# Kernel tuning notes

Hardware: AMD Instinct MI355X
Metric: run time of the kernel (lower is better)

The kernel has to match this reference:

```python
import jax, jax.numpy as jnp
import numpy as np

D_MODEL = 768
D_LAT = 384
N_FREQ = D_MODEL // 2 + 1  # 385
INIT_S = 0.02


def _quat_linear(x, Ww, Wx, Wy, Wz, b):
    # Ww..Wz: [out_q, in_q]; x: [..., 4*in_q]
    d = Ww.shape[1]
    xw, xx, xy, xz = x[..., :d], x[..., d:2*d], x[..., 2*d:3*d], x[..., 3*d:]
    lin = lambda W, v: jnp.einsum('...i,oi->...o', v, W)
    ow = lin(Ww, xw) - lin(Wx, xx) - lin(Wy, xy) - lin(Wz, xz)
    ox = lin(Ww, xx) + lin(Wx, xw) + lin(Wy, xz) - lin(Wz, xy)
    oy = lin(Ww, xy) - lin(Wx, xz) + lin(Wy, xw) + lin(Wz, xx)
    oz = lin(Ww, xz) + lin(Wx, xy) - lin(Wy, xx) + lin(Wz, xw)
    return jnp.concatenate([ow, ox, oy, oz], axis=-1) + b


def _filter1d(x, kr, ki, n):
    X = jnp.fft.rfft(x, axis=-1)
    K = kr + 1j * ki
    return jnp.fft.irfft(X * K, n=n, axis=-1)


def setup_inputs() -> dict:
    key = jax.random.key(0)
    ks = jax.random.split(key, 16)
    rn = lambda k, shape: jax.random.normal(k, shape, dtype=jnp.float32)
    in_q_e, out_q_e = D_MODEL // 4, D_LAT // 4   # 192, 96
    in_q_d, out_q_d = D_LAT // 4, D_MODEL // 4   # 96, 192
    return {
        'x': rn(ks[0], (8, 4096, D_MODEL)),
        'enc_kr': rn(ks[1], (N_FREQ,)) * INIT_S,
        'enc_ki': rn(ks[2], (N_FREQ,)) * INIT_S,
        'dec_kr': rn(ks[3], (N_FREQ,)) * INIT_S,
        'dec_ki': rn(ks[4], (N_FREQ,)) * INIT_S,
        'enc_Ww': rn(ks[5], (out_q_e, in_q_e)) * 0.02,
        'enc_Wx': rn(ks[6], (out_q_e, in_q_e)) * 0.02,
        'enc_Wy': rn(ks[7], (out_q_e, in_q_e)) * 0.02,
        'enc_Wz': rn(ks[8], (out_q_e, in_q_e)) * 0.02,
        'enc_b': jnp.zeros((D_LAT,), jnp.float32),
        'dec_Ww': rn(ks[9], (out_q_d, in_q_d)) * 0.02,
        'dec_Wx': rn(ks[10], (out_q_d, in_q_d)) * 0.02,
        'dec_Wy': rn(ks[11], (out_q_d, in_q_d)) * 0.02,
        'dec_Wz': rn(ks[12], (out_q_d, in_q_d)) * 0.02,
        'dec_b': jnp.zeros((D_MODEL,), jnp.float32),
    }


def reference(x, enc_kr, enc_ki, dec_kr, dec_ki,
              enc_Ww, enc_Wx, enc_Wy, enc_Wz, enc_b,
              dec_Ww, dec_Wx, dec_Wy, dec_Wz, dec_b):
    # encode: spectral filter -> GELU (exact erf, matching nn.GELU) -> quaternion proj
    h = jax.nn.gelu(_filter1d(x, enc_kr, enc_ki, D_MODEL), approximate=False)
    z = _quat_linear(h, enc_Ww, enc_Wx, enc_Wy, enc_Wz, enc_b)
    # decode: quaternion proj -> spectral filter
    recon = _filter1d(_quat_linear(z, dec_Ww, dec_Wx, dec_Wy, dec_Wz, dec_b),
                      dec_kr, dec_ki, D_MODEL)
    loss = jnp.mean((recon - jax.lax.stop_gradient(x)) ** 2)
    return z, loss
```

## Files before the change

### kernel.cpp

```cpp
#include <hip/hip_runtime.h>
#include <hip/hip_bf16.h>
#include <math.h>

typedef unsigned short u16;
typedef __attribute__((ext_vector_type(8))) short s8v;
typedef __attribute__((ext_vector_type(4))) float f4v;

#define DM 768
#define DL 384

__device__ __forceinline__ u16 f2bf(float f) {
  union { float f; unsigned u; } v; v.f = f;
  unsigned r = v.u + 0x7fffu + ((v.u >> 16) & 1u);
  return (u16)(r >> 16);
}

__global__ void k_build_c2(const float* __restrict__ kr0, const float* __restrict__ ki0,
                           const float* __restrict__ kr1, const float* __restrict__ ki1,
                           float* __restrict__ c0, float* __restrict__ c1) {
  const float* kr = blockIdx.y ? kr1 : kr0;
  const float* ki = blockIdx.y ? ki1 : ki0;
  float* c = blockIdx.y ? c1 : c0;
  const int t = blockIdx.x;
  const int f = threadIdx.x;
  float s = 0.f;
  for (int ff = f; ff < 384; ff += 256) {
    if (ff >= 1) {
      int ph = (ff * t) % DM;
      float th = (float)ph * (6.283185307179586f / DM);
      float sn, cs; sincosf(th, &sn, &cs);
      s += 2.f * (kr[ff] * cs - ki[ff] * sn);
    }
  }
  if (f == 0) s += kr[0] + ((t & 1) ? -kr[384] : kr[384]);
  __shared__ float red[256];
  red[f] = s; __syncthreads();
  for (int k = 128; k > 0; k >>= 1) {
    if (f < k) red[f] += red[f + k];
    __syncthreads();
  }
  if (f == 0) c[t] = red[0] * (1.f / DM);
}

__global__ void k_rb2(const float* __restrict__ c, const float* __restrict__ b,
                      float* __restrict__ rb) {
  const int i = blockIdx.x;
  const int f = threadIdx.x;
  float s = 0.f;
  for (int j = f; j < DM; j += 256) {
    int ci = i - j; if (ci < 0) ci += DM;
    s += c[ci] * b[j];
  }
  __shared__ float red[256];
  red[f] = s; __syncthreads();
  for (int k = 128; k > 0; k >>= 1) {
    if (f < k) red[f] += red[f + k];
    __syncthreads();
  }
  if (f == 0) rb[i] = red[0];
}

__device__ __constant__ int   MI_[4][4] = {{0,1,2,3},{1,0,3,2},{2,3,0,1},{3,2,1,0}};
__device__ __constant__ float SG_[4][4] = {{1,-1,-1,-1},{1,1,-1,1},{1,1,1,-1},{1,-1,1,1}};

__global__ void k_static(const float* __restrict__ c_enc, u16* __restrict__ Benc,
                         const float* __restrict__ c_dec, u16* __restrict__ Cdec,
                         const float* __restrict__ eWw, const float* __restrict__ eWx,
                         const float* __restrict__ eWy, const float* __restrict__ eWz,
                         u16* __restrict__ Wenc,
                         const float* __restrict__ dWw, const float* __restrict__ dWx,
                         const float* __restrict__ dWy, const float* __restrict__ dWz,
                         u16* __restrict__ DdT) {
  const int b = blockIdx.x;
  const int tt = threadIdx.x;
  if (b < 4608) {
    const float* c = (b < 2304) ? c_enc : c_dec;
    u16* B = (b < 2304) ? Benc : Cdec;
    int idx = (b < 2304 ? b : b - 2304) * 256 + tt;
    int i = idx / DM, j = idx % DM;
    int d = i - j; if (d < 0) d += DM;
    B[idx] = f2bf(c[d]);
  } else if (b < 5760) {
    int idx = (b - 4608) * 256 + tt;
    int o = idx / DM, j = idx % DM;
    int p = o / 96, r = o % 96, q = j / 192, cc = j % 192;
    const float* Ws[4] = {eWw, eWx, eWy, eWz};
    Wenc[idx] = f2bf(SG_[p][q] * Ws[MI_[p][q]][r * 192 + cc]);
  } else {
    int idx = (b - 5760) * 256 + tt;
    int o = idx / DM, j = idx % DM;
    int p = j / 192, r = j % 192, q = o / 96, cc = o % 96;
    const float* Ws[4] = {dWw, dWx, dWy, dWz};
    DdT[idx] = f2bf(SG_[p][q] * Ws[MI_[p][q]][r * 96 + cc]);
  }
}

__device__ __forceinline__ void ld_lds16(const u16* g, u16* l) {
  __builtin_amdgcn_global_load_lds((const __attribute__((address_space(1))) void*)g,
                                   (__attribute__((address_space(3))) void*)l, 16, 0, 0);
}

__global__ __launch_bounds__(512, 1) void gemm8f_g1(
    const float* __restrict__ X, const u16* __restrict__ B, u16* __restrict__ outb) {
  __shared__ __align__(16) u16 SM[57344];
  const int t = threadIdx.x;
  const int lane = t & 63, wid = t >> 6;
  const int wrow = wid >> 2, wcol = wid & 3;
  int wg = blockIdx.x;
  { const int q = gridDim.x >> 3; wg = (wg & 7) * q + (wg >> 3); }
  const int bm = wg >> 2, bn = wg & 3;
  constexpr int KT = 768, NT = 768, NKT = KT / 64;

  f4v acc[8][3];
#pragma unroll
  for (int m = 0; m < 8; ++m)
#pragma unroll
    for (int n = 0; n < 3; ++n) acc[m][n] = (f4v)0.f;

  const int srow = t >> 3;
  const int sgrp = (t & 7) ^ (srow & 7);
  const float* gX = X + (size_t)(bm * 256 + srow) * KT + sgrp * 8;
  const u16*   gB = B + (size_t)(bn * 192 + srow) * KT + sgrp * 8;
  const int sx = ((lane >> 4) ^ (lane & 7)) * 8;
  const int ar = (wrow * 128 + (lane & 15)) * 64;
  const int br = 32768 + (wcol * 48 + (lane & 15)) * 64;

  auto stgB = [&](int kt_, int c_) {
    const u16* g = gB + (size_t)(c_ * 64) * KT + kt_ * 64;
    ld_lds16(g, SM + 32768 + (kt_ & 1) * 12288 + c_ * 4096 + t * 8);
  };
  float4 ra0[4], ra1[4];
  auto LA = [&](int kt_, int half_, float4* r) {
    const float* g = gX + (size_t)(half_ * 128) * KT + kt_ * 64;
    r[0] = *(const float4*)(g);
    r[1] = *(const float4*)(g + 4);
    r[2] = *(const float4*)(g + 64 * KT);
    r[3] = *(const float4*)(g + 64 * KT + 4);
  };
  auto WA = [&](int kt_, int half_, const float4* r) {
    union { u16 u[8]; s8v s; } w0, w1;
    w0.u[0] = f2bf(r[0].x); w0.u[1] = f2bf(r[0].y);
    w0.u[2] = f2bf(r[0].z); w0.u[3] = f2bf(r[0].w);
    w0.u[4] = f2bf(r[1].x); w0.u[5] = f2bf(r[1].y);
    w0.u[6] = f2bf(r[1].z); w0.u[7] = f2bf(r[1].w);
    w1.u[0] = f2bf(r[2].x); w1.u[1] = f2bf(r[2].y);
    w1.u[2] = f2bf(r[2].z); w1.u[3] = f2bf(r[2].w);
    w1.u[4] = f2bf(r[3].x); w1.u[5] = f2bf(r[3].y);
    w1.u[6] = f2bf(r[3].z); w1.u[7] = f2bf(r[3].w);
    u16* l = SM + (kt_ & 1) * 16384 + half_ * 8192 + t * 8;
    *(s8v*)l = w0.s;
    *(s8v*)(l + 4096) = w1.s;
  };

  stgB(0, 0); stgB(0, 1); stgB(0, 2);
  LA(0, 0, ra0); LA(0, 1, ra1);
  asm volatile("s_waitcnt vmcnt(4)" ::: "memory");
  __builtin_amdgcn_sched_barrier(0);
  WA(0, 0, ra0);
  asm volatile("s_waitcnt vmcnt(0)" ::: "memory");
  __builtin_amdgcn_sched_barrier(0);
  WA(0, 1, ra1);
  asm volatile("s_waitcnt lgkmcnt(0)" ::: "memory");
  __builtin_amdgcn_sched_barrier(0);
  __builtin_amdgcn_s_barrier();

#pragma unroll 2
  for (int kt = 0; kt < NKT; ++kt) {
    const int ca = (kt & 1) * 16384;
    const int cbb = (kt & 1) * 12288;
    s8v a0[4][2], a1[4][2], b01[2][2], b2[2];
#pragma unroll
    for (int m = 0; m < 4; ++m) {
      a0[m][0] = *(const s8v*)(SM + ca + ar + m * 1024 + sx);
      a0[m][1] = *(const s8v*)(SM + ca + ar + m * 1024 + (sx ^ 32));
    }
#pragma unroll
    for (int n = 0; n < 2; ++n) {
      b01[n][0] = *(const s8v*)(SM + cbb + br + n * 1024 + sx);
      b01[n][1] = *(const s8v*)(SM + cbb + br + n * 1024 + (sx ^ 32));
    }
    if (kt + 1 < NKT) {
      stgB(kt + 1, 0); stgB(kt + 1, 1); stgB(kt + 1, 2);
      LA(kt + 1, 0, ra0);
      LA(kt + 1, 1, ra1);
    }
    __builtin_amdgcn_s_barrier();
    asm volatile("s_waitcnt lgkmcnt(0)" ::: "memory");
    __builtin_amdgcn_sched_barrier(0);
    __builtin_amdgcn_s_setprio(1);
#pragma unroll
    for (int m = 0; m < 4; ++m)
#pragma unroll
      for (int n = 0; n < 2; ++n) {
        acc[m][n] = __builtin_amdgcn_mfma_f32_16x16x32_bf16(a0[m][0], b01[n][0], acc[m][n], 0, 0, 0);
        acc[m][n] = __builtin_amdgcn_mfma_f32_16x16x32_bf16(a0[m][1], b01[n][1], acc[m][n], 0, 0, 0);
      }
    __builtin_amdgcn_s_setprio(0);
    __builtin_amdgcn_s_barrier();
#pragma unroll
    for (int m = 0; m < 4; ++m) {
      a1[m][0] = *(const s8v*)(SM + ca + ar + (4 + m) * 1024 + sx);
      a1[m][1] = *(const s8v*)(SM + ca + ar + (4 + m) * 1024 + (sx ^ 32));
    }
    __builtin_amdgcn_s_barrier();
    asm volatile("s_waitcnt lgkmcnt(0)" ::: "memory");
    __builtin_amdgcn_sched_barrier(0);
    __builtin_amdgcn_s_setprio(1);
#pragma unroll
    for (int m = 0; m < 4; ++m)
#pragma unroll
      for (int n = 0; n < 2; ++n) {
        acc[4 + m][n] = __builtin_amdgcn_mfma_f32_16x16x32_bf16(a1[m][0], b01[n][0], acc[4 + m][n], 0, 0, 0);
        acc[4 + m][n] = __builtin_amdgcn_mfma_f32_16x16x32_bf16(a1[m][1], b01[n][1], acc[4 + m][n], 0, 0, 0);
      }
    __builtin_amdgcn_s_setprio(0);
    __builtin_amdgcn_s_barrier();
    b2[0] = *(const s8v*)(SM + cbb + br + 2048 + sx);
    b2[1] = *(const s8v*)(SM + cbb + br + 2048 + (sx ^ 32));
    if (kt + 1 < NKT) {
      asm volatile("s_waitcnt vmcnt(4)" ::: "memory");
      __builtin_amdgcn_sched_barrier(0);
      WA(kt + 1, 0, ra0);
    }
    __builtin_amdgcn_s_barrier();
    asm volatile("s_waitcnt lgkmcnt(0)" ::: "memory");
    __builtin_amdgcn_sched_barrier(0);
    __builtin_amdgcn_s_setprio(1);
#pragma unroll
    for (int m = 0; m < 4; ++m) {
      acc[4 + m][2] = __builtin_amdgcn_mfma_f32_16x16x32_bf16(a1[m][0], b2[0], acc[4 + m][2], 0, 0, 0);
      acc[4 + m][2] = __builtin_amdgcn_mfma_f32_16x16x32_bf16(a1[m][1], b2[1], acc[4 + m][2], 0, 0, 0);
    }
    __builtin_amdgcn_s_setprio(0);
    __builtin_amdgcn_s_barrier();
    if (kt + 1 < NKT) {
      asm volatile("s_waitcnt vmcnt(0)" ::: "memory");
      __builtin_amdgcn_sched_barrier(0);
      WA(kt + 1, 1, ra1);
    }
    __builtin_amdgcn_s_barrier();
    asm volatile("s_waitcnt lgkmcnt(0)" ::: "memory");
    __builtin_amdgcn_sched_barrier(0);
    __builtin_amdgcn_s_setprio(1);
#pragma unroll
    for (int m = 0; m < 4; ++m) {
      acc[m][2] = __builtin_amdgcn_mfma_f32_16x16x32_bf16(a0[m][0], b2[0], acc[m][2], 0, 0, 0);
      acc[m][2] = __builtin_amdgcn_mfma_f32_16x16x32_bf16(a0[m][1], b2[1], acc[m][2], 0, 0, 0);
    }
    __builtin_amdgcn_s_setprio(0);
    __builtin_amdgcn_s_barrier();
  }

  for (int ch = 0; ch < 2; ++ch) {
    if (wrow == ch) {
#pragma unroll
      for (int m = 0; m < 8; ++m)
#pragma unroll
        for (int n = 0; n < 3; ++n)
#pragma unroll
          for (int j = 0; j < 4; ++j) {
            float v = acc[m][n][j];
            float u = v * 0.70710678118f, u2 = u * u;
            float p = u * (1.1283791671f + u2 * (-0.37612638903f +
                      u2 * (0.11283791671f + u2 * (-0.02686617064f))));
            v = 0.5f * v * (1.f + p);
            SM[(m * 16 + (lane >> 4) * 4 + j) * 200 + wcol * 48 + n * 16 + (lane & 15)] = f2bf(v);
          }
    }
    __syncthreads();
#pragma unroll
    for (int it = 0; it < 6; ++it) {
      int idx = it * 512 + t;
      int r = idx / 24, c8 = (idx % 24) * 8;
      s8v vv = *(const s8v*)(SM + r * 200 + c8);
      *(s8v*)(outb + (size_t)(bm * 256 + ch * 128 + r) * NT + bn * 192 + c8) = vv;
    }
    __syncthreads();
  }
}

template <int KT, int NT, int NBN, int EPI, int SWZ>
__global__ __launch_bounds__(256, 3) void gemm_ring(
    const u16* __restrict__ A, const u16* __restrict__ B,
    u16* __restrict__ outb, float* __restrict__ outf,
    const float* __restrict__ bias, const float* __restrict__ xref,
    float* __restrict__ partials) {
  __shared__ __align__(16) u16 SMR[24576];
#define As_(b) (SMR + (b) * 4096)
#define Bs_(b) (SMR + 12288 + (b) * 4096)
  const int t = threadIdx.x;
  const int wid = t >> 6, lane = t & 63;
  const int wr = wid >> 1, wc = wid & 1;
  int wg = blockIdx.x;
  if (SWZ) { const int q = gridDim.x >> 3; wg = (wg & 7) * q + (wg >> 3); }
  const int bm = wg / NBN, bn = wg % NBN;

  f4v acc[4][4];
#pragma unroll
  for (int m = 0; m < 4; ++m)
#pragma unroll
    for (int n = 0; n < 4; ++n) acc[m][n] = (f4v)0.f;

  const int sgo = ((t & 3) ^ ((t >> 3) & 3)) * 8;
  const u16* gA = A + (size_t)(bm * 128 + (t >> 2)) * KT + sgo;
  const u16* gB = B + (size_t)(bn * 128 + (t >> 2)) * KT + sgo;
  const int fr = lane & 15;
  const int fo = ((lane >> 4) ^ ((fr >> 1) & 3)) * 8;
  constexpr int NK = KT / 32;

  auto stage = [&](int kt_, int b_) {
    const int ko = kt_ * 32;
    ld_lds16(gA + ko, As_(b_) + wid * 512);
    ld_lds16(gA + ko + 64 * KT, As_(b_) + wid * 512 + 2048);
    ld_lds16(gB + ko, Bs_(b_) + wid * 512);
    ld_lds16(gB + ko + 64 * KT, Bs_(b_) + wid * 512 + 2048);
  };

  stage(0, 0);
  stage(1, 1);
#pragma unroll 3
  for (int kt = 0; kt < NK; ++kt) {
    const int b0 = kt % 3, b2 = (kt + 2) % 3;
    if (kt + 2 < NK) stage(kt + 2, b2);
    const int ahead = NK - 1 - kt;
    if (ahead >= 2)      { asm volatile("s_waitcnt vmcnt(8)" ::: "memory"); }
    else if (ahead == 1) { asm volatile("s_waitcnt vmcnt(4)" ::: "memory"); }
    else                 { asm volatile("s_waitcnt vmcnt(0)" ::: "memory"); }
    __builtin_amdgcn_sched_barrier(0);
    __builtin_amdgcn_s_barrier();
    s8v af[4], bfv[4];
#pragma unroll
    for (int m = 0; m < 4; ++m)
      af[m] = *(const s8v*)(As_(b0) + (wr * 64 + m * 16 + fr) * 32 + fo);
#pragma unroll
    for (int n = 0; n < 4; ++n)
      bfv[n] = *(const s8v*)(Bs_(b0) + (wc * 64 + n * 16 + fr) * 32 + fo);
    asm volatile("s_waitcnt lgkmcnt(0)" ::: "memory");
    __builtin_amdgcn_sched_barrier(0);
    __builtin_amdgcn_s_barrier();
    __builtin_amdgcn_s_setprio(1);
#pragma unroll
    for (int m = 0; m < 4; ++m)
#pragma unroll
      for (int n = 0; n < 4; ++n)
        acc[m][n] = __builtin_amdgcn_mfma_f32_16x16x32_bf16(af[m], bfv[n], acc[m][n], 0, 0, 0);
    __builtin_amdgcn_s_setprio(0);
  }

  const int r0l = wr * 64 + ((lane >> 4) << 2);
  const int c0l = wc * 64 + (lane & 15);

  if constexpr (EPI == 2) {
    float bc[4];
#pragma unroll
    for (int n = 0; n < 4; ++n) bc[n] = bias[bn * 128 + c0l + n * 16];
    float ls = 0.f;
#pragma unroll
    for (int m = 0; m < 4; ++m)
#pragma unroll
      for (int n = 0; n < 4; ++n)
#pragma unroll
        for (int j = 0; j < 4; ++j) {
          size_t row = bm * 128 + r0l + m * 16 + j;
          int col = bn * 128 + c0l + n * 16;
          float v = acc[m][n][j] + bc[n];
          float d = v - xref[row * NT + col];
          ls += d * d;
        }
#pragma unroll
    for (int o = 32; o > 0; o >>= 1) ls += __shfl_down(ls, o);
    float* rw = (float*)SMR;
    if (lane == 0) rw[wid] = ls;
    __syncthreads();
    if (t == 0) partials[blockIdx.x] = rw[0] + rw[1] + rw[2] + rw[3];
  } else {
    u16* Cs = SMR;
    float bc[4];
    if constexpr (EPI == 1) {
#pragma unroll
      for (int n = 0; n < 4; ++n) bc[n] = bias[bn * 128 + c0l + n * 16];
    }
#pragma unroll
    for (int m = 0; m < 4; ++m)
#pragma unroll
      for (int n = 0; n < 4; ++n)
#pragma unroll
        for (int j = 0; j < 4; ++j) {
          float v = acc[m][n][j];
          if constexpr (EPI == 1) {
            v += bc[n];
            outf[(size_t)(bm * 128 + r0l + m * 16 + j) * NT + bn * 128 + c0l + n * 16] = v;
          }
          Cs[(r0l + m * 16 + j) * 130 + c0l + n * 16] = f2bf(v);
        }
    __syncthreads();
#pragma unroll
    for (int s = 0; s < 8; ++s) {
      int idx = (s * 256 + t) * 8;
      int r = idx >> 7, c = idx & 127;
      s8v vv = *(const s8v*)(Cs + r * 130 + c);
      *(s8v*)(outb + (size_t)(bm * 128 + r) * NT + bn * 128 + c) = vv;
    }
  }
#undef As_
#undef Bs_
}

__global__ void k_loss_final(const float* __restrict__ partials, float* __restrict__ out) {
  __shared__ float red[256];
  float s = 0.f;
  for (int i = threadIdx.x; i < 1536; i += 256) s += partials[i];
  red[threadIdx.x] = s; __syncthreads();
  for (int k = 128; k > 0; k >>= 1) {
    if (threadIdx.x < k) red[threadIdx.x] += red[threadIdx.x + k];
    __syncthreads();
  }
  if (threadIdx.x == 0) out[0] = red[0] / 25165824.f;
}

extern "C" void kernel_launch(void* const* d_in, const int* in_sizes, int n_in,
                              void* d_out, int out_size, void* d_ws, size_t ws_size,
                              hipStream_t stream) {
  const float* x      = (const float*)d_in[0];
  const float* enc_kr = (const float*)d_in[1];
  const float* enc_ki = (const float*)d_in[2];
  const float* dec_kr = (const float*)d_in[3];
  const float* dec_ki = (const float*)d_in[4];
  const float* enc_Ww = (const float*)d_in[5];
  const float* enc_Wx = (const float*)d_in[6];
  const float* enc_Wy = (const float*)d_in[7];
  const float* enc_Wz = (const float*)d_in[8];
  const float* enc_b  = (const float*)d_in[9];
  const float* dec_Ww = (const float*)d_in[10];
  const float* dec_Wx = (const float*)d_in[11];
  const float* dec_Wy = (const float*)d_in[12];
  const float* dec_Wz = (const float*)d_in[13];
  const float* dec_b  = (const float*)d_in[14];

  char* ws = (char*)d_ws;
  float* c_enc    = (float*)(ws + 0);
  float* c_dec    = (float*)(ws + 4096);
  float* rb       = (float*)(ws + 8192);
  float* partials = (float*)(ws + 12288);
  u16*   Benc     = (u16*)(ws + 20480);
  u16*   Wenc     = (u16*)(ws + 1200128);
  u16*   Mdec     = (u16*)(ws + 1789952);
  u16*   Cdec     = (u16*)(ws + 2379776);
  u16*   DdT      = (u16*)(ws + 3559424);
  u16*   Zb       = (u16*)(ws + 4149248);
  u16*   H        = (u16*)(ws + 29315072);

  k_build_c2<<<dim3(768, 2), 256, 0, stream>>>(enc_kr, enc_ki, dec_kr, dec_ki, c_enc, c_dec);
  k_rb2<<<768, 256, 0, stream>>>(c_dec, dec_b, rb);
  k_static<<<6912, 256, 0, stream>>>(c_enc, Benc, c_dec, Cdec,
                                     enc_Ww, enc_Wx, enc_Wy, enc_Wz, Wenc,
                                     dec_Ww, dec_Wx, dec_Wy, dec_Wz, DdT);
  gemm_ring<768, 384, 3, 3, 0><<<18, 256, 0, stream>>>(Cdec, DdT, Mdec, nullptr, nullptr, nullptr, nullptr);

  float* zout = (float*)d_out;
  gemm8f_g1<<<512, 512, 0, stream>>>(x, Benc, H);
  gemm_ring<768, 384, 3, 1, 1><<<768, 256, 0, stream>>>(H, Wenc, Zb, zout, enc_b, nullptr, nullptr);
  gemm_ring<384, 768, 6, 2, 1><<<1536, 256, 0, stream>>>(Zb, Mdec, nullptr, nullptr, rb, x, partials);
  k_loss_final<<<1, 256, 0, stream>>>(partials, zout + (out_size - 1));
}
```

Baseline: 157.5 us.

## Halve M tile of first GEMM and restructure its pipeline for higher occupancy

The fused fp32-to-bf16 spectral filter GEMM now uses a 128x192 tile instead of 256x192, with half the accumulators and LDS. Launch bounds rise to allow several blocks per CU, and the grid doubles to 1024 blocks. The K loop is rescheduled so A fp32 loads are prefetched two steps ahead, with B fragments loaded per column group. The aim is better latency hiding through occupancy and a less serialized schedule. The cost is lower per-block reuse of B and more global traffic for B.

```diff
diff --git a/kernel.cpp b/kernel.cpp
--- a/kernel.cpp
+++ b/kernel.cpp
@@ -100,161 +100,134 @@
                                    (__attribute__((address_space(3))) void*)l, 16, 0, 0);
 }
 
-__global__ __launch_bounds__(512, 1) void gemm8f_g1(
+__global__ __launch_bounds__(512, 4) void gemm3p_g1(
     const float* __restrict__ X, const u16* __restrict__ B, u16* __restrict__ outb) {
-  __shared__ __align__(16) u16 SM[57344];
+  __shared__ __align__(16) u16 SM[40960];
   const int t = threadIdx.x;
   const int lane = t & 63, wid = t >> 6;
   const int wrow = wid >> 2, wcol = wid & 3;
+  const int qg = lane >> 4, fr = lane & 15;
   int wg = blockIdx.x;
   { const int q = gridDim.x >> 3; wg = (wg & 7) * q + (wg >> 3); }
   const int bm = wg >> 2, bn = wg & 3;
   constexpr int KT = 768, NT = 768, NKT = KT / 64;
 
-  f4v acc[8][3];
-#pragma unroll
-  for (int m = 0; m < 8; ++m)
+  f4v acc[4][3];
+#pragma unroll
+  for (int m = 0; m < 4; ++m)
 #pragma unroll
     for (int n = 0; n < 3; ++n) acc[m][n] = (f4v)0.f;
 
   const int srow = t >> 3;
   const int sgrp = (t & 7) ^ (srow & 7);
-  const float* gX = X + (size_t)(bm * 256 + srow) * KT + sgrp * 8;
+  const float* gX = X + (size_t)(bm * 128 + srow) * KT + sgrp * 8;
   const u16*   gB = B + (size_t)(bn * 192 + srow) * KT + sgrp * 8;
-  const int sx = ((lane >> 4) ^ (lane & 7)) * 8;
-  const int ar = (wrow * 128 + (lane & 15)) * 64;
-  const int br = 32768 + (wcol * 48 + (lane & 15)) * 64;
+  const int sx = (qg ^ (lane & 7)) * 8;
+  const int ar = (wrow * 64 + fr) * 64;
+  const int br = 16384 + (wcol * 48 + fr) * 64;
 
   auto stgB = [&](int kt_, int c_) {
     const u16* g = gB + (size_t)(c_ * 64) * KT + kt_ * 64;
-    ld_lds16(g, SM + 32768 + (kt_ & 1) * 12288 + c_ * 4096 + t * 8);
+    ld_lds16(g, SM + 16384 + (kt_ & 1) * 12288 + c_ * 4096 + t * 8);
   };
-  float4 ra0[4], ra1[4];
-  auto LA = [&](int kt_, int half_, float4* r) {
-    const float* g = gX + (size_t)(half_ * 128) * KT + kt_ * 64;
-    r[0] = *(const float4*)(g);
-    r[1] = *(const float4*)(g + 4);
-    r[2] = *(const float4*)(g + 64 * KT);
-    r[3] = *(const float4*)(g + 64 * KT + 4);
+  float4 ra[4];
+  auto LA = [&](int kt_) {
+    const float* g = gX + kt_ * 64;
+    ra[0] = *(const float4*)(g);
+    ra[1] = *(const float4*)(g + 4);
+    ra[2] = *(const float4*)(g + 64 * KT);
+    ra[3] = *(const float4*)(g + 64 * KT + 4);
   };
-  auto WA = [&](int kt_, int half_, const float4* r) {
+  auto WA = [&](int kt_) {
     union { u16 u[8]; s8v s; } w0, w1;
-    w0.u[0] = f2bf(r[0].x); w0.u[1] = f2bf(r[0].y);
-    w0.u[2] = f2bf(r[0].z); w0.u[3] = f2bf(r[0].w);
-    w0.u[4] = f2bf(r[1].x); w0.u[5] = f2bf(r[1].y);
-    w0.u[6] = f2bf(r[1].z); w0.u[7] = f2bf(r[1].w);
-    w1.u[0] = f2bf(r[2].x); w1.u[1] = f2bf(r[2].y);
-    w1.u[2] = f2bf(r[2].z); w1.u[3] = f2bf(r[2].w);
-    w1.u[4] = f2bf(r[3].x); w1.u[5] = f2bf(r[3].y);
-    w1.u[6] = f2bf(r[3].z); w1.u[7] = f2bf(r[3].w);
-    u16* l = SM + (kt_ & 1) * 16384 + half_ * 8192 + t * 8;
+    w0.u[0] = f2bf(ra[0].x); w0.u[1] = f2bf(ra[0].y);
+    w0.u[2] = f2bf(ra[0].z); w0.u[3] = f2bf(ra[0].w);
+    w0.u[4] = f2bf(ra[1].x); w0.u[5] = f2bf(ra[1].y);
+    w0.u[6] = f2bf(ra[1].z); w0.u[7] = f2bf(ra[1].w);
+    w1.u[0] = f2bf(ra[2].x); w1.u[1] = f2bf(ra[2].y);
+    w1.u[2] = f2bf(ra[2].z); w1.u[3] = f2bf(ra[2].w);
+    w1.u[4] = f2bf(ra[3].x); w1.u[5] = f2bf(ra[3].y);
+    w1.u[6] = f2bf(ra[3].z); w1.u[7] = f2bf(ra[3].w);
+    u16* l = SM + (kt_ & 1) * 8192 + t * 8;
     *(s8v*)l = w0.s;
     *(s8v*)(l + 4096) = w1.s;
   };
 
   stgB(0, 0); stgB(0, 1); stgB(0, 2);
-  LA(0, 0, ra0); LA(0, 1, ra1);
-  asm volatile("s_waitcnt vmcnt(4)" ::: "memory");
-  __builtin_amdgcn_sched_barrier(0);
-  WA(0, 0, ra0);
+  LA(0);
   asm volatile("s_waitcnt vmcnt(0)" ::: "memory");
   __builtin_amdgcn_sched_barrier(0);
-  WA(0, 1, ra1);
+  WA(0);
+  LA(1);
   asm volatile("s_waitcnt lgkmcnt(0)" ::: "memory");
   __builtin_amdgcn_sched_barrier(0);
   __builtin_amdgcn_s_barrier();
 
 #pragma unroll 2
   for (int kt = 0; kt < NKT; ++kt) {
-    const int ca = (kt & 1) * 16384;
+    const int ca = (kt & 1) * 8192;
     const int cbb = (kt & 1) * 12288;
-    s8v a0[4][2], a1[4][2], b01[2][2], b2[2];
+    s8v a[4][2], bf[2];
 #pragma unroll
     for (int m = 0; m < 4; ++m) {
-      a0[m][0] = *(const s8v*)(SM + ca + ar + m * 1024 + sx);
-      a0[m][1] = *(const s8v*)(SM + ca + ar + m * 1024 + (sx ^ 32));
-    }
-#pragma unroll
-    for (int n = 0; n < 2; ++n) {
-      b01[n][0] = *(const s8v*)(SM + cbb + br + n * 1024 + sx);
-      b01[n][1] = *(const s8v*)(SM + cbb + br + n * 1024 + (sx ^ 32));
-    }
+      a[m][0] = *(const s8v*)(SM + ca + ar + m * 1024 + sx);
+      a[m][1] = *(const s8v*)(SM + ca + ar + m * 1024 + (sx ^ 32));
+    }
+    bf[0] = *(const s8v*)(SM + cbb + br + sx);
+    bf[1] = *(const s8v*)(SM + cbb + br + (sx ^ 32));
     if (kt + 1 < NKT) {
       stgB(kt + 1, 0); stgB(kt + 1, 1); stgB(kt + 1, 2);
-      LA(kt + 1, 0, ra0);
-      LA(kt + 1, 1, ra1);
+      asm volatile("s_waitcnt vmcnt(3)" ::: "memory");
+      __builtin_amdgcn_sched_barrier(0);
+      WA(kt + 1);
     }
     __builtin_amdgcn_s_barrier();
     asm volatile("s_waitcnt lgkmcnt(0)" ::: "memory");
     __builtin_amdgcn_sched_barrier(0);
     __builtin_amdgcn_s_setprio(1);
 #pragma unroll
-    for (int m = 0; m < 4; ++m)
-#pragma unroll
-      for (int n = 0; n < 2; ++n) {
-        acc[m][n] = __builtin_amdgcn_mfma_f32_16x16x32_bf16(a0[m][0], b01[n][0], acc[m][n], 0, 0, 0);
-        acc[m][n] = __builtin_amdgcn_mfma_f32_16x16x32_bf16(a0[m][1], b01[n][1], acc[m][n], 0, 0, 0);
-      }
+    for (int m = 0; m < 4; ++m) {
+      acc[m][0] = __builtin_amdgcn_mfma_f32_16x16x32_bf16(a[m][0], bf[0], acc[m][0], 0, 0, 0);
+      acc[m][0] = __builtin_amdgcn_mfma_f32_16x16x32_bf16(a[m][1], bf[1], acc[m][0], 0, 0, 0);
+    }
     __builtin_amdgcn_s_setprio(0);
     __builtin_amdgcn_s_barrier();
+    bf[0] = *(const s8v*)(SM + cbb + br + 1024 + sx);
+    bf[1] = *(const s8v*)(SM + cbb + br + 1024 + (sx ^ 32));
+    if (kt + 2 < NKT) LA(kt + 2);
+    __builtin_amdgcn_s_barrier();
+    asm volatile("s_waitcnt lgkmcnt(0)" ::: "memory");
+    __builtin_amdgcn_sched_barrier(0);
+    __builtin_amdgcn_s_setprio(1);
 #pragma unroll
     for (int m = 0; m < 4; ++m) {
-      a1[m][0] = *(const s8v*)(SM + ca + ar + (4 + m) * 1024 + sx);
-      a1[m][1] = *(const s8v*)(SM + ca + ar + (4 + m) * 1024 + (sx ^ 32));
-    }
+      acc[m][1] = __builtin_amdgcn_mfma_f32_16x16x32_bf16(a[m][0], bf[0], acc[m][1], 0, 0, 0);
+      acc[m][1] = __builtin_amdgcn_mfma_f32_16x16x32_bf16(a[m][1], bf[1], acc[m][1], 0, 0, 0);
+    }
+    __builtin_amdgcn_s_setprio(0);
+    __builtin_amdgcn_s_barrier();
+    bf[0] = *(const s8v*)(SM + cbb + br + 2048 + sx);
+    bf[1] = *(const s8v*)(SM + cbb + br + 2048 + (sx ^ 32));
     __builtin_amdgcn_s_barrier();
     asm volatile("s_waitcnt lgkmcnt(0)" ::: "memory");
     __builtin_amdgcn_sched_barrier(0);
     __builtin_amdgcn_s_setprio(1);
 #pragma unroll
-    for (int m = 0; m < 4; ++m)
-#pragma unroll
-      for (int n = 0; n < 2; ++n) {
-        acc[4 + m][n] = __builtin_amdgcn_mfma_f32_16x16x32_bf16(a1[m][0], b01[n][0], acc[4 + m][n], 0, 0, 0);
-        acc[4 + m][n] = __builtin_amdgcn_mfma_f32_16x16x32_bf16(a1[m][1], b01[n][1], acc[4 + m][n], 0, 0, 0);
-      }
+    for (int m = 0; m < 4; ++m) {
+      acc[m][2] = __builtin_amdgcn_mfma_f32_16x16x32_bf16(a[m][0], bf[0], acc[m][2], 0, 0, 0);
+      acc[m][2] = __builtin_amdgcn_mfma_f32_16x16x32_bf16(a[m][1], bf[1], acc[m][2], 0, 0, 0);
+    }
     __builtin_amdgcn_s_setprio(0);
-    __builtin_amdgcn_s_barrier();
-    b2[0] = *(const s8v*)(SM + cbb + br + 2048 + sx);
-    b2[1] = *(const s8v*)(SM + cbb + br + 2048 + (sx ^ 32));
-    if (kt + 1 < NKT) {
-      asm volatile("s_waitcnt vmcnt(4)" ::: "memory");
-      __builtin_amdgcn_sched_barrier(0);
-      WA(kt + 1, 0, ra0);
-    }
-    __builtin_amdgcn_s_barrier();
-    asm volatile("s_waitcnt lgkmcnt(0)" ::: "memory");
-    __builtin_amdgcn_sched_barrier(0);
-    __builtin_amdgcn_s_setprio(1);
-#pragma unroll
-    for (int m = 0; m < 4; ++m) {
-      acc[4 + m][2] = __builtin_amdgcn_mfma_f32_16x16x32_bf16(a1[m][0], b2[0], acc[4 + m][2], 0, 0, 0);
-      acc[4 + m][2] = __builtin_amdgcn_mfma_f32_16x16x32_bf16(a1[m][1], b2[1], acc[4 + m][2], 0, 0, 0);
-    }
-    __builtin_amdgcn_s_setprio(0);
-    __builtin_amdgcn_s_barrier();
-    if (kt + 1 < NKT) {
-      asm volatile("s_waitcnt vmcnt(0)" ::: "memory");
-      __builtin_amdgcn_sched_barrier(0);
-      WA(kt + 1, 1, ra1);
-    }
-    __builtin_amdgcn_s_barrier();
-    asm volatile("s_waitcnt lgkmcnt(0)" ::: "memory");
-    __builtin_amdgcn_sched_barrier(0);
-    __builtin_amdgcn_s_setprio(1);
-#pragma unroll
-    for (int m = 0; m < 4; ++m) {
-      acc[m][2] = __builtin_amdgcn_mfma_f32_16x16x32_bf16(a0[m][0], b2[0], acc[m][2], 0, 0, 0);
-      acc[m][2] = __builtin_amdgcn_mfma_f32_16x16x32_bf16(a0[m][1], b2[1], acc[m][2], 0, 0, 0);
-    }
-    __builtin_amdgcn_s_setprio(0);
+    if (kt + 2 < NKT)      { asm volatile("s_waitcnt vmcnt(4)" ::: "memory"); }
+    else if (kt + 1 < NKT) { asm volatile("s_waitcnt vmcnt(0)" ::: "memory"); }
+    __builtin_amdgcn_sched_barrier(0);
     __builtin_amdgcn_s_barrier();
   }
 
   for (int ch = 0; ch < 2; ++ch) {
     if (wrow == ch) {
 #pragma unroll
-      for (int m = 0; m < 8; ++m)
+      for (int m = 0; m < 4; ++m)
 #pragma unroll
         for (int n = 0; n < 3; ++n)
 #pragma unroll
@@ -264,16 +237,16 @@
             float p = u * (1.1283791671f + u2 * (-0.37612638903f +
                       u2 * (0.11283791671f + u2 * (-0.02686617064f))));
             v = 0.5f * v * (1.f + p);
-            SM[(m * 16 + (lane >> 4) * 4 + j) * 200 + wcol * 48 + n * 16 + (lane & 15)] = f2bf(v);
+            SM[(m * 16 + qg * 4 + j) * 200 + wcol * 48 + n * 16 + fr] = f2bf(v);
           }
     }
     __syncthreads();
 #pragma unroll
-    for (int it = 0; it < 6; ++it) {
+    for (int it = 0; it < 3; ++it) {
       int idx = it * 512 + t;
       int r = idx / 24, c8 = (idx % 24) * 8;
       s8v vv = *(const s8v*)(SM + r * 200 + c8);
-      *(s8v*)(outb + (size_t)(bm * 256 + ch * 128 + r) * NT + bn * 192 + c8) = vv;
+      *(s8v*)(outb + (size_t)(bm * 128 + ch * 64 + r) * NT + bn * 192 + c8) = vv;
     }
     __syncthreads();
   }
@@ -458,7 +431,7 @@
   gemm_ring<768, 384, 3, 3, 0><<<18, 256, 0, stream>>>(Cdec, DdT, Mdec, nullptr, nullptr, nullptr, nullptr);
 
   float* zout = (float*)d_out;
-  gemm8f_g1<<<512, 512, 0, stream>>>(x, Benc, H);
+  gemm3p_g1<<<1024, 512, 0, stream>>>(x, Benc, H);
   gemm_ring<768, 384, 3, 1, 1><<<768, 256, 0, stream>>>(H, Wenc, Zb, zout, enc_b, nullptr, nullptr);
   gemm_ring<384, 768, 6, 2, 1><<<1536, 256, 0, stream>>>(Zb, Mdec, nullptr, nullptr, rb, x, partials);
   k_loss_final<<<1, 256, 0, stream>>>(partials, zout + (out_size - 1));
```

Result: slower. 162.9 us (+3.4%).

## Fold bias-convolution into static kernel, stagger A loads, use intrinsic bf16 convert

Applied to the files above, without the earlier changes.

Removes the separate k_rb2 launch by computing the decoder bias circular convolution in three extra blocks of k_static, each thread doing a serial 768-term loop. In the main fp32-to-bf16 GEMM, the second half of the next A tile is now loaded after the first MFMA phase instead of with the first half, spreading register pressure and memory issue across the iteration. The manual bf16 rounding is replaced by the HIP intrinsic conversion. The serial per-thread reduction is slower per element but runs in parallel with other static blocks, and the moved load leaves less time to hide its latency.

```diff
diff --git a/kernel.cpp b/kernel.cpp
--- a/kernel.cpp
+++ b/kernel.cpp
@@ -13,6 +13,9 @@
   union { float f; unsigned u; } v; v.f = f;
   unsigned r = v.u + 0x7fffu + ((v.u >> 16) & 1u);
   return (u16)(r >> 16);
+}
+__device__ __forceinline__ u16 f2bf_rne(float f) {
+  return __bfloat16_as_ushort(__float2bfloat16(f));
 }
 
 __global__ void k_build_c2(const float* __restrict__ kr0, const float* __restrict__ ki0,
@@ -42,24 +45,6 @@
   if (f == 0) c[t] = red[0] * (1.f / DM);
 }
 
-__global__ void k_rb2(const float* __restrict__ c, const float* __restrict__ b,
-                      float* __restrict__ rb) {
-  const int i = blockIdx.x;
-  const int f = threadIdx.x;
-  float s = 0.f;
-  for (int j = f; j < DM; j += 256) {
-    int ci = i - j; if (ci < 0) ci += DM;
-    s += c[ci] * b[j];
-  }
-  __shared__ float red[256];
-  red[f] = s; __syncthreads();
-  for (int k = 128; k > 0; k >>= 1) {
-    if (f < k) red[f] += red[f + k];
-    __syncthreads();
-  }
-  if (f == 0) rb[i] = red[0];
-}
-
 __device__ __constant__ int   MI_[4][4] = {{0,1,2,3},{1,0,3,2},{2,3,0,1},{3,2,1,0}};
 __device__ __constant__ float SG_[4][4] = {{1,-1,-1,-1},{1,1,-1,1},{1,1,1,-1},{1,-1,1,1}};
 
@@ -70,7 +55,8 @@
                          u16* __restrict__ Wenc,
                          const float* __restrict__ dWw, const float* __restrict__ dWx,
                          const float* __restrict__ dWy, const float* __restrict__ dWz,
-                         u16* __restrict__ DdT) {
+                         u16* __restrict__ DdT,
+                         const float* __restrict__ dec_b, float* __restrict__ rb) {
   const int b = blockIdx.x;
   const int tt = threadIdx.x;
   if (b < 4608) {
@@ -86,12 +72,18 @@
     int p = o / 96, r = o % 96, q = j / 192, cc = j % 192;
     const float* Ws[4] = {eWw, eWx, eWy, eWz};
     Wenc[idx] = f2bf(SG_[p][q] * Ws[MI_[p][q]][r * 192 + cc]);
-  } else {
+  } else if (b < 6912) {
     int idx = (b - 5760) * 256 + tt;
     int o = idx / DM, j = idx % DM;
     int p = j / 192, r = j % 192, q = o / 96, cc = o % 96;
     const float* Ws[4] = {dWw, dWx, dWy, dWz};
     DdT[idx] = f2bf(SG_[p][q] * Ws[MI_[p][q]][r * 96 + cc]);
+  } else {
+    const int i = (b - 6912) * 256 + 0;
+    int row = (b - 6912) * 256 + tt;
+    float s = 0.f; int ci = row;
+    for (int j = 0; j < DM; ++j) { s += c_dec[ci] * dec_b[j]; ci = ci ? ci - 1 : DM - 1; }
+    rb[row] = s;
   }
 }
 
@@ -139,14 +131,14 @@
   };
   auto WA = [&](int kt_, int half_, const float4* r) {
     union { u16 u[8]; s8v s; } w0, w1;
-    w0.u[0] = f2bf(r[0].x); w0.u[1] = f2bf(r[0].y);
-    w0.u[2] = f2bf(r[0].z); w0.u[3] = f2bf(r[0].w);
-    w0.u[4] = f2bf(r[1].x); w0.u[5] = f2bf(r[1].y);
-    w0.u[6] = f2bf(r[1].z); w0.u[7] = f2bf(r[1].w);
-    w1.u[0] = f2bf(r[2].x); w1.u[1] = f2bf(r[2].y);
-    w1.u[2] = f2bf(r[2].z); w1.u[3] = f2bf(r[2].w);
-    w1.u[4] = f2bf(r[3].x); w1.u[5] = f2bf(r[3].y);
-    w1.u[6] = f2bf(r[3].z); w1.u[7] = f2bf(r[3].w);
+    w0.u[0] = f2bf_rne(r[0].x); w0.u[1] = f2bf_rne(r[0].y);
+    w0.u[2] = f2bf_rne(r[0].z); w0.u[3] = f2bf_rne(r[0].w);
+    w0.u[4] = f2bf_rne(r[1].x); w0.u[5] = f2bf_rne(r[1].y);
+    w0.u[6] = f2bf_rne(r[1].z); w0.u[7] = f2bf_rne(r[1].w);
+    w1.u[0] = f2bf_rne(r[2].x); w1.u[1] = f2bf_rne(r[2].y);
+    w1.u[2] = f2bf_rne(r[2].z); w1.u[3] = f2bf_rne(r[2].w);
+    w1.u[4] = f2bf_rne(r[3].x); w1.u[5] = f2bf_rne(r[3].y);
+    w1.u[6] = f2bf_rne(r[3].z); w1.u[7] = f2bf_rne(r[3].w);
     u16* l = SM + (kt_ & 1) * 16384 + half_ * 8192 + t * 8;
     *(s8v*)l = w0.s;
     *(s8v*)(l + 4096) = w1.s;
@@ -182,7 +174,6 @@
     if (kt + 1 < NKT) {
       stgB(kt + 1, 0); stgB(kt + 1, 1); stgB(kt + 1, 2);
       LA(kt + 1, 0, ra0);
-      LA(kt + 1, 1, ra1);
     }
     __builtin_amdgcn_s_barrier();
     asm volatile("s_waitcnt lgkmcnt(0)" ::: "memory");
@@ -202,6 +193,7 @@
       a1[m][0] = *(const s8v*)(SM + ca + ar + (4 + m) * 1024 + sx);
       a1[m][1] = *(const s8v*)(SM + ca + ar + (4 + m) * 1024 + (sx ^ 32));
     }
+    if (kt + 1 < NKT) LA(kt + 1, 1, ra1);
     __builtin_amdgcn_s_barrier();
     asm volatile("s_waitcnt lgkmcnt(0)" ::: "memory");
     __builtin_amdgcn_sched_barrier(0);
@@ -451,10 +443,10 @@
   u16*   H        = (u16*)(ws + 29315072);
 
   k_build_c2<<<dim3(768, 2), 256, 0, stream>>>(enc_kr, enc_ki, dec_kr, dec_ki, c_enc, c_dec);
-  k_rb2<<<768, 256, 0, stream>>>(c_dec, dec_b, rb);
-  k_static<<<6912, 256, 0, stream>>>(c_enc, Benc, c_dec, Cdec,
+  k_static<<<6915, 256, 0, stream>>>(c_enc, Benc, c_dec, Cdec,
                                      enc_Ww, enc_Wx, enc_Wy, enc_Wz, Wenc,
-                                     dec_Ww, dec_Wx, dec_Wy, dec_Wz, DdT);
+                                     dec_Ww, dec_Wx, dec_Wy, dec_Wz, DdT,
+                                     dec_b, rb);
   gemm_ring<768, 384, 3, 3, 0><<<18, 256, 0, stream>>>(Cdec, DdT, Mdec, nullptr, nullptr, nullptr, nullptr);
 
   float* zout = (float*)d_out;
```

New measurement: 174.5 us. 10.8% more time.
